# Optimization experiments

Measured on AMD Instinct MI355X. Metric: run time of the kernel, lower is better.

## Reference

```python
import jax, jax.numpy as jnp
import numpy as np

N = 50000      # nodes
E = 600000     # edges (avg degree 12)
D = 128        # input_dim == hidden_dim (required: same Linear reused across pool layers)
OUT = 64       # output_dim
NUM_POOL = 2   # num_pool_layers


def setup_inputs() -> dict:
    key = jax.random.key(0)
    ks = jax.random.split(key, 8)
    s = 1.0 / np.sqrt(D)  # fan-in style scaling keeps repeated scatter-adds stable
    x = jax.random.normal(ks[0], (N, D), dtype=jnp.float32)
    edge_index = jax.random.randint(ks[1], (2, E), 0, N, dtype=jnp.int64)
    W1 = jax.random.normal(ks[2], (D, D), dtype=jnp.float32) * s
    b1 = jnp.zeros((D,), dtype=jnp.float32)
    W2 = jax.random.normal(ks[3], (D, D), dtype=jnp.float32) * s
    b2 = jnp.zeros((D,), dtype=jnp.float32)
    Wout = jax.random.normal(ks[4], (D, OUT), dtype=jnp.float32) * s
    bout = jnp.zeros((OUT,), dtype=jnp.float32)
    return {"x": x, "edge_index": edge_index, "W1": W1, "b1": b1,
            "W2": W2, "b2": b2, "Wout": Wout, "bout": bout}


def _gauss_seidel_pool(x, W, b, src, dst, num_layers):
    # PyG MessagePassing(aggr='add'): out[i] = sum_{edges (j->i)} lin(x[j]).
    # Nodes with no incoming edges become zero (propagate replaces x entirely).
    for _ in range(num_layers):
        m = x @ W + b                      # [N, out] linear once per node (== lin(x_j) per edge)
        x = jax.ops.segment_sum(m[src], dst, num_segments=N)  # gather + scatter-add
    return x


def reference(x, edge_index, W1, b1, W2, b2, Wout, bout):
    src = edge_index[0]  # x_j source
    dst = edge_index[1]  # aggregation target i
    h = _gauss_seidel_pool(x, W1, b1, src, dst, NUM_POOL)
    h = jax.nn.relu(h)                     # dropout = identity (eval mode)
    h = _gauss_seidel_pool(h, W2, b2, src, dst, NUM_POOL)
    h = jax.nn.relu(h)
    return h @ Wout + bout                 # [N, OUT]
```

## Files before the change

kernel.cpp:

```cpp
#include <hip/hip_runtime.h>


static inline int ceil_div(int a, int b) { return (a + b - 1) / b; }

typedef __attribute__((ext_vector_type(8))) short bf16x8;
typedef __attribute__((ext_vector_type(4))) float f32x4;

__device__ inline unsigned short f2bf(float f) {
    unsigned u = __float_as_uint(f);
    return (unsigned short)((u + 0x7fffu + ((u >> 16) & 1u)) >> 16);
}
__device__ inline float bf2f(unsigned short h) {
    return __uint_as_float(((unsigned)h) << 16);
}


__device__ void wprep_dev(const float* __restrict__ W, unsigned short* __restrict__ hi,
                          unsigned short* __restrict__ lo, int total, int C,
                          int g0, int G) {
    for (int t = g0; t < total; t += G) {
        int j = t & 7;
        int lane = (t >> 3) & 63;
        int f = t >> 9;
        int c = f & 3, ct = f >> 2;
        int k = c * 32 + (lane >> 4) * 8 + j;
        int col = ct * 16 + (lane & 15);
        float w = W[(size_t)k * C + col];
        unsigned short h = f2bf(w);
        hi[t] = h;
        lo[t] = f2bf(w - bf2f(h));
    }
}

__global__ __launch_bounds__(256) void prep_kernel(const float* __restrict__ W1,
                                                   const float* __restrict__ W2,
                                                   const float* __restrict__ Wout,
                                                   unsigned short* __restrict__ W1hi,
                                                   unsigned short* __restrict__ W1lo,
                                                   unsigned short* __restrict__ W2hi,
                                                   unsigned short* __restrict__ W2lo,
                                                   unsigned short* __restrict__ Wohi,
                                                   unsigned short* __restrict__ Wolo,
                                                   int* __restrict__ cursor, int N) {
    int g0 = blockIdx.x * 256 + threadIdx.x;
    int G = gridDim.x * 256;
    for (int i = g0; i < N; i += G) cursor[i] = 0;
    wprep_dev(W1, W1hi, W1lo, 128 * 128, 128, g0, G);
    wprep_dev(W2, W2hi, W2lo, 128 * 128, 128, g0, G);
    wprep_dev(Wout, Wohi, Wolo, 128 * 64, 64, g0, G);
}


__global__ __launch_bounds__(256) void hist_kernel(const int* __restrict__ dst,
                                                   int* __restrict__ deg, int E) {
    int e = blockIdx.x * 256 + threadIdx.x;
    if (e < E) atomicAdd(&deg[dst[e]], 1);
}

__global__ __launch_bounds__(256) void scan_blocks_kernel(const int* __restrict__ deg,
                                                          int* __restrict__ rp,
                                                          int* __restrict__ partials,
                                                          int n, int N) {
    __shared__ int s[256];
    int tid = threadIdx.x;
    int i = blockIdx.x * 256 + tid;
    int v = (i < N) ? deg[i] : 0;
    s[tid] = v;
    __syncthreads();
    for (int off = 1; off < 256; off <<= 1) {
        int t = (tid >= off) ? s[tid - off] : 0;
        __syncthreads();
        s[tid] += t;
        __syncthreads();
    }
    if (i < n) rp[i] = s[tid] - v;
    if (tid == 255) partials[blockIdx.x] = s[255];
}

__global__ __launch_bounds__(256) void add_offsets2_kernel(int* __restrict__ rp,
                                                           const int* __restrict__ partials,
                                                           int* __restrict__ cursor,
                                                           int N) {
    __shared__ int s[256];
    int c = blockIdx.x, tid = threadIdx.x;
    s[tid] = (tid < c) ? partials[tid] : 0;
    __syncthreads();
    for (int off = 128; off >= 1; off >>= 1) {
        if (tid < off) s[tid] += s[tid + off];
        __syncthreads();
    }
    int prefix = s[0];
    int i = c * 256 + tid;
    if (i <= N) {
        int v = rp[i] + prefix;
        rp[i] = v;
        if (i < N) cursor[i] = v;
    }
}

__global__ __launch_bounds__(256) void fill_kernel(const int* __restrict__ src,
                                                   const int* __restrict__ dst,
                                                   int* __restrict__ cursor,
                                                   int* __restrict__ es, int E) {
    int e = blockIdx.x * 256 + threadIdx.x;
    if (e < E) {
        int p = atomicAdd(&cursor[dst[e]], 1);
        es[p] = src[e];
    }
}


__global__ __launch_bounds__(256) void gemm1_kernel(const float* __restrict__ X,
                                                    const uint4* __restrict__ Whi,
                                                    const uint4* __restrict__ Wlo,
                                                    const float* __restrict__ Bias,
                                                    unsigned short* __restrict__ Y, int n) {
    int tid = threadIdx.x;
    int wave = tid >> 6, lane = tid & 63;
    int lm = lane & 15, lq = lane >> 4;
    int r0 = blockIdx.x * 64;

    bf16x8 afr[4][4];
#pragma unroll
    for (int rt = 0; rt < 4; ++rt) {
        int ar = r0 + rt * 16 + lm;
        if (ar > n - 1) ar = n - 1;
#pragma unroll
        for (int c = 0; c < 4; ++c) {
            int k = c * 32 + lq * 8;
            const float* ap = X + (size_t)ar * 128 + k;
            float4 f0 = ((const float4*)ap)[0];
            float4 f1 = ((const float4*)ap)[1];
            bf16x8 v;
            v[0] = (short)f2bf(f0.x); v[1] = (short)f2bf(f0.y);
            v[2] = (short)f2bf(f0.z); v[3] = (short)f2bf(f0.w);
            v[4] = (short)f2bf(f1.x); v[5] = (short)f2bf(f1.y);
            v[6] = (short)f2bf(f1.z); v[7] = (short)f2bf(f1.w);
            afr[rt][c] = v;
        }
    }

    f32x4 acc[4][2];
#pragma unroll
    for (int rt = 0; rt < 4; ++rt)
#pragma unroll
        for (int t = 0; t < 2; ++t)
            acc[rt][t] = (f32x4){0.f, 0.f, 0.f, 0.f};

#pragma unroll
    for (int c = 0; c < 4; ++c) {
#pragma unroll
        for (int t = 0; t < 2; ++t) {
            int ct = wave * 2 + t;
            uint4 uh = Whi[(ct * 4 + c) * 64 + lane];
            uint4 ul = Wlo[(ct * 4 + c) * 64 + lane];
            bf16x8 wh = *(const bf16x8*)&uh;
            bf16x8 wl = *(const bf16x8*)&ul;
#pragma unroll
            for (int rt = 0; rt < 4; ++rt) {
                acc[rt][t] = __builtin_amdgcn_mfma_f32_16x16x32_bf16(afr[rt][c], wh, acc[rt][t], 0, 0, 0);
                acc[rt][t] = __builtin_amdgcn_mfma_f32_16x16x32_bf16(afr[rt][c], wl, acc[rt][t], 0, 0, 0);
            }
        }
    }

#pragma unroll
    for (int t = 0; t < 2; ++t) {
        int col = (wave * 2 + t) * 16 + lm;
        float bias = Bias[col];
#pragma unroll
        for (int rt = 0; rt < 4; ++rt) {
#pragma unroll
            for (int r = 0; r < 4; ++r) {
                int row = r0 + rt * 16 + lq * 4 + r;
                if (row < n)
                    Y[(size_t)row * 128 + col] = f2bf(acc[rt][t][r] + bias);
            }
        }
    }
}


__device__ inline void acc_row8(float* a, uint4 v) {
    a[0] += __uint_as_float(v.x << 16);
    a[1] += __uint_as_float(v.x & 0xffff0000u);
    a[2] += __uint_as_float(v.y << 16);
    a[3] += __uint_as_float(v.y & 0xffff0000u);
    a[4] += __uint_as_float(v.z << 16);
    a[5] += __uint_as_float(v.z & 0xffff0000u);
    a[6] += __uint_as_float(v.w << 16);
    a[7] += __uint_as_float(v.w & 0xffff0000u);
}

template <int COLS, bool OUTF32>
__global__ __launch_bounds__(256) void fused_agg_gemm_kernel(const unsigned short* __restrict__ M,
                                                             const int* __restrict__ rp,
                                                             const int* __restrict__ es,
                                                             const uint4* __restrict__ Whi,
                                                             const uint4* __restrict__ Wlo,
                                                             const float* __restrict__ Bias,
                                                             void* __restrict__ Yv,
                                                             int n, int do_relu) {
    constexpr int CT_W = COLS / 64;
    constexpr int SR = 136;
    __shared__ unsigned short Hl[64 * SR];

    int tid = threadIdx.x;
    int r0 = blockIdx.x * 64;

    {
        int sub = tid >> 4, ln = tid & 15;
        for (int q = 0; q < 4; ++q) {
            int nl = sub * 4 + q;
            int node = r0 + nl;
            float acc[8] = {};
            if (node < n) {
                int beg = rp[node], end = rp[node + 1];
                int e = beg;
                for (; e + 4 <= end; e += 4) {
                    int s0 = es[e], s1 = es[e + 1], s2 = es[e + 2], s3 = es[e + 3];
                    uint4 v0 = ((const uint4*)(M + (size_t)s0 * 128))[ln];
                    uint4 v1 = ((const uint4*)(M + (size_t)s1 * 128))[ln];
                    uint4 v2 = ((const uint4*)(M + (size_t)s2 * 128))[ln];
                    uint4 v3 = ((const uint4*)(M + (size_t)s3 * 128))[ln];
                    acc_row8(acc, v0);
                    acc_row8(acc, v1);
                    acc_row8(acc, v2);
                    acc_row8(acc, v3);
                }
                for (; e < end; ++e) {
                    uint4 v = ((const uint4*)(M + (size_t)es[e] * 128))[ln];
                    acc_row8(acc, v);
                }
                if (do_relu) {
#pragma unroll
                    for (int i = 0; i < 8; ++i) acc[i] = fmaxf(acc[i], 0.f);
                }
            }
            uint4 o;
            o.x = (unsigned)f2bf(acc[0]) | ((unsigned)f2bf(acc[1]) << 16);
            o.y = (unsigned)f2bf(acc[2]) | ((unsigned)f2bf(acc[3]) << 16);
            o.z = (unsigned)f2bf(acc[4]) | ((unsigned)f2bf(acc[5]) << 16);
            o.w = (unsigned)f2bf(acc[6]) | ((unsigned)f2bf(acc[7]) << 16);
            *(uint4*)(&Hl[nl * SR + ln * 8]) = o;
        }
    }
    __syncthreads();

    int wave = tid >> 6, lane = tid & 63;
    int lm = lane & 15, lq = lane >> 4;

    f32x4 acc[4][CT_W];
#pragma unroll
    for (int rt = 0; rt < 4; ++rt)
#pragma unroll
        for (int t = 0; t < CT_W; ++t)
            acc[rt][t] = (f32x4){0.f, 0.f, 0.f, 0.f};

#pragma unroll
    for (int c = 0; c < 4; ++c) {
        bf16x8 afr[4];
#pragma unroll
        for (int rt = 0; rt < 4; ++rt) {
            int nl = rt * 16 + lm;
            afr[rt] = *(const bf16x8*)(&Hl[nl * SR + c * 32 + lq * 8]);
        }
#pragma unroll
        for (int t = 0; t < CT_W; ++t) {
            int ct = wave * CT_W + t;
            uint4 uh = Whi[(ct * 4 + c) * 64 + lane];
            uint4 ul = Wlo[(ct * 4 + c) * 64 + lane];
            bf16x8 wh = *(const bf16x8*)&uh;
            bf16x8 wl = *(const bf16x8*)&ul;
#pragma unroll
            for (int rt = 0; rt < 4; ++rt) {
                acc[rt][t] = __builtin_amdgcn_mfma_f32_16x16x32_bf16(afr[rt], wh, acc[rt][t], 0, 0, 0);
                acc[rt][t] = __builtin_amdgcn_mfma_f32_16x16x32_bf16(afr[rt], wl, acc[rt][t], 0, 0, 0);
            }
        }
    }

#pragma unroll
    for (int t = 0; t < CT_W; ++t) {
        int col = (wave * CT_W + t) * 16 + lm;
        float bias = Bias[col];
#pragma unroll
        for (int rt = 0; rt < 4; ++rt) {
#pragma unroll
            for (int r = 0; r < 4; ++r) {
                int row = r0 + rt * 16 + lq * 4 + r;
                if (row < n) {
                    float v = acc[rt][t][r] + bias;
                    if (OUTF32)
                        ((float*)Yv)[(size_t)row * COLS + col] = v;
                    else
                        ((unsigned short*)Yv)[(size_t)row * COLS + col] = f2bf(v);
                }
            }
        }
    }
}


extern "C" void kernel_launch(void* const* d_in, const int* in_sizes, int n_in,
                              void* d_out, int out_size, void* d_ws, size_t ws_size,
                              hipStream_t stream) {
    const float* x    = (const float*)d_in[0];
    const int*   ei   = (const int*)d_in[1];
    const float* W1   = (const float*)d_in[2];
    const float* b1   = (const float*)d_in[3];
    const float* W2   = (const float*)d_in[4];
    const float* b2   = (const float*)d_in[5];
    const float* Wout = (const float*)d_in[6];
    const float* bout = (const float*)d_in[7];
    float*       out  = (float*)d_out;

    const int N = in_sizes[0] / 128;
    const int E = in_sizes[1] / 2;
    const int* src = ei;
    const int* dst = ei + E;

    char* ws = (char*)d_ws;
    auto take = [&](size_t bytes) {
        char* p = ws;
        ws += (bytes + 255) & ~(size_t)255;
        return p;
    };
    unsigned short* mA = (unsigned short*)take((size_t)N * 128 * 2);
    unsigned short* mB = (unsigned short*)take((size_t)N * 128 * 2);
    unsigned short* W1hi = (unsigned short*)take(128 * 128 * 2);
    unsigned short* W1lo = (unsigned short*)take(128 * 128 * 2);
    unsigned short* W2hi = (unsigned short*)take(128 * 128 * 2);
    unsigned short* W2lo = (unsigned short*)take(128 * 128 * 2);
    unsigned short* Wohi = (unsigned short*)take(128 * 64 * 2);
    unsigned short* Wolo = (unsigned short*)take(128 * 64 * 2);
    int* rp      = (int*)take((size_t)(N + 1) * sizeof(int));
    int* cursor  = (int*)take((size_t)N * sizeof(int));
    int* es      = (int*)take((size_t)E * sizeof(int));
    int* partials = (int*)take(4096);

    prep_kernel<<<256, 256, 0, stream>>>(W1, W2, Wout, W1hi, W1lo, W2hi, W2lo,
                                         Wohi, Wolo, cursor, N);
    hist_kernel<<<ceil_div(E, 256), 256, 0, stream>>>(dst, cursor, E);
    int nChunks = ceil_div(N + 1, 256);
    scan_blocks_kernel<<<nChunks, 256, 0, stream>>>(cursor, rp, partials, N + 1, N);
    add_offsets2_kernel<<<nChunks, 256, 0, stream>>>(rp, partials, cursor, N);
    fill_kernel<<<ceil_div(E, 256), 256, 0, stream>>>(src, dst, cursor, es, E);

    const int tiles = ceil_div(N, 64);

    gemm1_kernel<<<tiles, 256, 0, stream>>>(x, (const uint4*)W1hi, (const uint4*)W1lo,
                                            b1, mA, N);
    fused_agg_gemm_kernel<128, false><<<tiles, 256, 0, stream>>>(
        mA, rp, es, (const uint4*)W1hi, (const uint4*)W1lo, b1, mB, N, 0);
    fused_agg_gemm_kernel<128, false><<<tiles, 256, 0, stream>>>(
        mB, rp, es, (const uint4*)W2hi, (const uint4*)W2lo, b2, mA, N, 1);
    fused_agg_gemm_kernel<128, false><<<tiles, 256, 0, stream>>>(
        mA, rp, es, (const uint4*)W2hi, (const uint4*)W2lo, b2, mB, N, 0);
    fused_agg_gemm_kernel<64, true><<<tiles, 256, 0, stream>>>(
        mB, rp, es, (const uint4*)Wohi, (const uint4*)Wolo, bout, out, N, 1);
}
```

Measured before the change: 302.8 us.

## Drop bf16 lo-split weights, fuse scan passes and fill with first GEMM

Weights are now kept only as a single bf16 copy, which halves the MFMA work and the weight loads in every GEMM. The cost is lower accuracy than the hi+lo split used before. The two-pass block scan becomes one kernel that chains across blocks using spin-waiting on per-block status flags. The CSR fill is merged into the first GEMM launch as extra blocks, which removes several kernel launches. The spin-wait assumes earlier blocks get scheduled, which holds for about 196 blocks.

Result: no change. 299.4 us (-1.1%).

```diff
diff --git a/kernel.cpp b/kernel.cpp
--- a/kernel.cpp
+++ b/kernel.cpp
@@ -10,14 +10,10 @@
     unsigned u = __float_as_uint(f);
     return (unsigned short)((u + 0x7fffu + ((u >> 16) & 1u)) >> 16);
 }
-__device__ inline float bf2f(unsigned short h) {
-    return __uint_as_float(((unsigned)h) << 16);
-}
 
 
 __device__ void wprep_dev(const float* __restrict__ W, unsigned short* __restrict__ hi,
-                          unsigned short* __restrict__ lo, int total, int C,
-                          int g0, int G) {
+                          int total, int C, int g0, int G) {
     for (int t = g0; t < total; t += G) {
         int j = t & 7;
         int lane = (t >> 3) & 63;
@@ -25,10 +21,7 @@
         int c = f & 3, ct = f >> 2;
         int k = c * 32 + (lane >> 4) * 8 + j;
         int col = ct * 16 + (lane & 15);
-        float w = W[(size_t)k * C + col];
-        unsigned short h = f2bf(w);
-        hi[t] = h;
-        lo[t] = f2bf(w - bf2f(h));
+        hi[t] = f2bf(W[(size_t)k * C + col]);
     }
 }
 
@@ -36,18 +29,18 @@
                                                    const float* __restrict__ W2,
                                                    const float* __restrict__ Wout,
                                                    unsigned short* __restrict__ W1hi,
-                                                   unsigned short* __restrict__ W1lo,
                                                    unsigned short* __restrict__ W2hi,
-                                                   unsigned short* __restrict__ W2lo,
                                                    unsigned short* __restrict__ Wohi,
-                                                   unsigned short* __restrict__ Wolo,
-                                                   int* __restrict__ cursor, int N) {
+                                                   int* __restrict__ cursor,
+                                                   unsigned* __restrict__ stat,
+                                                   int N, int nChunks) {
     int g0 = blockIdx.x * 256 + threadIdx.x;
     int G = gridDim.x * 256;
     for (int i = g0; i < N; i += G) cursor[i] = 0;
-    wprep_dev(W1, W1hi, W1lo, 128 * 128, 128, g0, G);
-    wprep_dev(W2, W2hi, W2lo, 128 * 128, 128, g0, G);
-    wprep_dev(Wout, Wohi, Wolo, 128 * 64, 64, g0, G);
+    for (int i = g0; i < nChunks; i += G) stat[i] = 0;
+    wprep_dev(W1, W1hi, 128 * 128, 128, g0, G);
+    wprep_dev(W2, W2hi, 128 * 128, 128, g0, G);
+    wprep_dev(Wout, Wohi, 128 * 64, 64, g0, G);
 }
 
 
@@ -57,13 +50,14 @@
     if (e < E) atomicAdd(&deg[dst[e]], 1);
 }
 
-__global__ __launch_bounds__(256) void scan_blocks_kernel(const int* __restrict__ deg,
-                                                          int* __restrict__ rp,
-                                                          int* __restrict__ partials,
-                                                          int n, int N) {
+__global__ __launch_bounds__(256) void scan_fuse_kernel(const int* __restrict__ deg,
+                                                        int* __restrict__ rp,
+                                                        int* __restrict__ cursor,
+                                                        unsigned* __restrict__ stat,
+                                                        int N) {
     __shared__ int s[256];
-    int tid = threadIdx.x;
-    int i = blockIdx.x * 256 + tid;
+    int c = blockIdx.x, tid = threadIdx.x;
+    int i = c * 256 + tid;
     int v = (i < N) ? deg[i] : 0;
     s[tid] = v;
     __syncthreads();
@@ -73,52 +67,54 @@
         s[tid] += t;
         __syncthreads();
     }
-    if (i < n) rp[i] = s[tid] - v;
-    if (tid == 255) partials[blockIdx.x] = s[255];
-}
-
-__global__ __launch_bounds__(256) void add_offsets2_kernel(int* __restrict__ rp,
-                                                           const int* __restrict__ partials,
-                                                           int* __restrict__ cursor,
-                                                           int N) {
-    __shared__ int s[256];
-    int c = blockIdx.x, tid = threadIdx.x;
-    s[tid] = (tid < c) ? partials[tid] : 0;
+    int loc = s[tid] - v;
+    int tot = s[255];
+    __syncthreads();
+    if (tid == 0) atomicExch(&stat[c], (unsigned)tot | 0x80000000u);
+
+    unsigned mine = 0;
+    if (tid < c) {
+        unsigned u;
+        do { u = atomicAdd(&stat[tid], 0u); } while (!(u & 0x80000000u));
+        mine = u & 0x7fffffffu;
+    }
+    s[tid] = (int)mine;
     __syncthreads();
     for (int off = 128; off >= 1; off >>= 1) {
         if (tid < off) s[tid] += s[tid + off];
         __syncthreads();
     }
     int prefix = s[0];
-    int i = c * 256 + tid;
     if (i <= N) {
-        int v = rp[i] + prefix;
-        rp[i] = v;
-        if (i < N) cursor[i] = v;
-    }
-}
-
-__global__ __launch_bounds__(256) void fill_kernel(const int* __restrict__ src,
-                                                   const int* __restrict__ dst,
-                                                   int* __restrict__ cursor,
-                                                   int* __restrict__ es, int E) {
-    int e = blockIdx.x * 256 + threadIdx.x;
-    if (e < E) {
-        int p = atomicAdd(&cursor[dst[e]], 1);
-        es[p] = src[e];
-    }
-}
-
-
-__global__ __launch_bounds__(256) void gemm1_kernel(const float* __restrict__ X,
-                                                    const uint4* __restrict__ Whi,
-                                                    const uint4* __restrict__ Wlo,
-                                                    const float* __restrict__ Bias,
-                                                    unsigned short* __restrict__ Y, int n) {
+        int val = loc + prefix;
+        rp[i] = val;
+        if (i < N) cursor[i] = val;
+    }
+}
+
+
+__global__ __launch_bounds__(256) void fill_gemm1_kernel(const int* __restrict__ src,
+                                                         const int* __restrict__ dst,
+                                                         int* __restrict__ cursor,
+                                                         int* __restrict__ es, int E,
+                                                         const float* __restrict__ X,
+                                                         const uint4* __restrict__ Whi,
+                                                         const float* __restrict__ Bias,
+                                                         unsigned short* __restrict__ Y,
+                                                         int n, int fillB) {
     int tid = threadIdx.x;
+    if ((int)blockIdx.x < fillB) {
+        int e = blockIdx.x * 256 + tid;
+        if (e < E) {
+            int p = atomicAdd(&cursor[dst[e]], 1);
+            es[p] = src[e];
+        }
+        return;
+    }
+
+    int r0 = (blockIdx.x - fillB) * 64;
     int wave = tid >> 6, lane = tid & 63;
     int lm = lane & 15, lq = lane >> 4;
-    int r0 = blockIdx.x * 64;
 
     bf16x8 afr[4][4];
 #pragma unroll
@@ -153,14 +149,10 @@
         for (int t = 0; t < 2; ++t) {
             int ct = wave * 2 + t;
             uint4 uh = Whi[(ct * 4 + c) * 64 + lane];
-            uint4 ul = Wlo[(ct * 4 + c) * 64 + lane];
             bf16x8 wh = *(const bf16x8*)&uh;
-            bf16x8 wl = *(const bf16x8*)&ul;
-#pragma unroll
-            for (int rt = 0; rt < 4; ++rt) {
+#pragma unroll
+            for (int rt = 0; rt < 4; ++rt)
                 acc[rt][t] = __builtin_amdgcn_mfma_f32_16x16x32_bf16(afr[rt][c], wh, acc[rt][t], 0, 0, 0);
-                acc[rt][t] = __builtin_amdgcn_mfma_f32_16x16x32_bf16(afr[rt][c], wl, acc[rt][t], 0, 0, 0);
-            }
         }
     }
 
@@ -197,7 +189,6 @@
                                                              const int* __restrict__ rp,
                                                              const int* __restrict__ es,
                                                              const uint4* __restrict__ Whi,
-                                                             const uint4* __restrict__ Wlo,
                                                              const float* __restrict__ Bias,
                                                              void* __restrict__ Yv,
                                                              int n, int do_relu) {
@@ -269,14 +260,10 @@
         for (int t = 0; t < CT_W; ++t) {
             int ct = wave * CT_W + t;
             uint4 uh = Whi[(ct * 4 + c) * 64 + lane];
-            uint4 ul = Wlo[(ct * 4 + c) * 64 + lane];
             bf16x8 wh = *(const bf16x8*)&uh;
-            bf16x8 wl = *(const bf16x8*)&ul;
-#pragma unroll
-            for (int rt = 0; rt < 4; ++rt) {
+#pragma unroll
+            for (int rt = 0; rt < 4; ++rt)
                 acc[rt][t] = __builtin_amdgcn_mfma_f32_16x16x32_bf16(afr[rt], wh, acc[rt][t], 0, 0, 0);
-                acc[rt][t] = __builtin_amdgcn_mfma_f32_16x16x32_bf16(afr[rt], wl, acc[rt][t], 0, 0, 0);
-            }
         }
     }
 
@@ -329,34 +316,31 @@
     unsigned short* mA = (unsigned short*)take((size_t)N * 128 * 2);
     unsigned short* mB = (unsigned short*)take((size_t)N * 128 * 2);
     unsigned short* W1hi = (unsigned short*)take(128 * 128 * 2);
-    unsigned short* W1lo = (unsigned short*)take(128 * 128 * 2);
     unsigned short* W2hi = (unsigned short*)take(128 * 128 * 2);
-    unsigned short* W2lo = (unsigned short*)take(128 * 128 * 2);
     unsigned short* Wohi = (unsigned short*)take(128 * 64 * 2);
-    unsigned short* Wolo = (unsigned short*)take(128 * 64 * 2);
     int* rp      = (int*)take((size_t)(N + 1) * sizeof(int));
     int* cursor  = (int*)take((size_t)N * sizeof(int));
     int* es      = (int*)take((size_t)E * sizeof(int));
-    int* partials = (int*)take(4096);
-
-    prep_kernel<<<256, 256, 0, stream>>>(W1, W2, Wout, W1hi, W1lo, W2hi, W2lo,
-                                         Wohi, Wolo, cursor, N);
+    unsigned* stat = (unsigned*)take(4096);
+
+    const int nChunks = ceil_div(N + 1, 256);
+    const int tiles = ceil_div(N, 64);
+    const int fillB = ceil_div(E, 256);
+
+    prep_kernel<<<256, 256, 0, stream>>>(W1, W2, Wout, W1hi, W2hi, Wohi,
+                                         cursor, stat, N, nChunks);
     hist_kernel<<<ceil_div(E, 256), 256, 0, stream>>>(dst, cursor, E);
-    int nChunks = ceil_div(N + 1, 256);
-    scan_blocks_kernel<<<nChunks, 256, 0, stream>>>(cursor, rp, partials, N + 1, N);
-    add_offsets2_kernel<<<nChunks, 256, 0, stream>>>(rp, partials, cursor, N);
-    fill_kernel<<<ceil_div(E, 256), 256, 0, stream>>>(src, dst, cursor, es, E);
-
-    const int tiles = ceil_div(N, 64);
-
-    gemm1_kernel<<<tiles, 256, 0, stream>>>(x, (const uint4*)W1hi, (const uint4*)W1lo,
-                                            b1, mA, N);
+    scan_fuse_kernel<<<nChunks, 256, 0, stream>>>(cursor, rp, cursor, stat, N);
+    fill_gemm1_kernel<<<fillB + tiles, 256, 0, stream>>>(src, dst, cursor, es, E,
+                                                         x, (const uint4*)W1hi, b1,
+                                                         mA, N, fillB);
+
     fused_agg_gemm_kernel<128, false><<<tiles, 256, 0, stream>>>(
-        mA, rp, es, (const uint4*)W1hi, (const uint4*)W1lo, b1, mB, N, 0);
+        mA, rp, es, (const uint4*)W1hi, b1, mB, N, 0);
     fused_agg_gemm_kernel<128, false><<<tiles, 256, 0, stream>>>(
-        mB, rp, es, (const uint4*)W2hi, (const uint4*)W2lo, b2, mA, N, 1);
+        mB, rp, es, (const uint4*)W2hi, b2, mA, N, 1);
     fused_agg_gemm_kernel<128, false><<<tiles, 256, 0, stream>>>(
-        mA, rp, es, (const uint4*)W2hi, (const uint4*)W2lo, b2, mB, N, 0);
+        mA, rp, es, (const uint4*)W2hi, b2, mB, N, 0);
     fused_agg_gemm_kernel<64, true><<<tiles, 256, 0, stream>>>(
-        mB, rp, es, (const uint4*)Wohi, (const uint4*)Wolo, bout, out, N, 1);
-}
+        mB, rp, es, (const uint4*)Wohi, bout, out, N, 1);
+}
```
